# Performance work log

Measured on AMD Instinct MI355X. Metric: run time of the kernel, lower is better.

The kernel has to match this reference:

```python
import jax, jax.numpy as jnp
import numpy as np

V, D, M, R = 100000, 256, 8192, 32
B_SZ, L = 2048, 100


def setup_inputs() -> dict:
    key = jax.random.key(0)
    k1, k2, k3, k4 = jax.random.split(key, 4)
    ids = jax.random.randint(k1, (B_SZ, L), 0, V, dtype=jnp.int64)
    idx = jnp.arange(M, dtype=jnp.int64)  # unique adapter row ids
    E = jax.random.normal(k2, (V, D), dtype=jnp.float32)
    A_rows = jax.random.normal(k3, (M, R), dtype=jnp.float32) * (1.0 / np.sqrt(R))
    Bm = jax.random.normal(k4, (D, R), dtype=jnp.float32) * (1.0 / np.sqrt(R))
    return {"ids": ids, "idx": idx, "E": E, "A_rows": A_rows, "B": Bm}


def reference(ids, idx, E, A_rows, B):
    # base embedding gather: [B, L, D]
    base = E[ids]
    # Equivalent to the one-hot matmul (idx unique): map each vocab id to its
    # adapter-row position, -1 if not adapted.
    pos = jnp.full((V,), -1, dtype=jnp.int32).at[idx].set(
        jnp.arange(idx.shape[0], dtype=jnp.int32))
    p = pos[ids]                      # [B, L]
    hit = (p >= 0)[..., None]         # [B, L, 1]
    A_sel = jnp.where(hit, A_rows[jnp.clip(p, 0)], 0.0)  # [B, L, R]
    delta = jnp.einsum('blr,dr->bld', A_sel, B)           # [B, L, D]
    return base + delta
```

## Files before the change

kernel.cpp:

```cpp
#include <hip/hip_runtime.h>

#define V_SZ   100000
#define D_SZ   256
#define M_SZ   8192
#define R_SZ   32
#define NTOK   (2048 * 100)
#define TPW    8

typedef float f4_t __attribute__((ext_vector_type(4)));

__global__ __launch_bounds__(256) void build_kernel(
    const int*   __restrict__ idx,
    int*         __restrict__ pos,
    const float* __restrict__ E,
    const float* __restrict__ A_rows,
    const float* __restrict__ Bm,
    float*       __restrict__ D2) {

    __shared__ float BtL[R_SZ * D_SZ];

    const int tid = threadIdx.x;

    const int gid = blockIdx.x * 256 + tid;
    if (gid < M_SZ) pos[idx[gid]] = gid;

    for (int f = tid; f < D_SZ * R_SZ; f += 256) {
        BtL[(f & (R_SZ - 1)) * D_SZ + (f >> 5)] = Bm[f];
    }
    __syncthreads();

    const int lane  = tid & 63;
    const int wv    = __builtin_amdgcn_readfirstlane(tid >> 6);
    const int dofs  = lane * 4;
    const int mbase = blockIdx.x * 16 + wv * 4;

    #pragma unroll
    for (int k = 0; k < 4; ++k) {
        const int m   = mbase + k;
        const int row = idx[m];
        const float4 e = *(const float4*)(E + (size_t)row * D_SZ + dofs);
        float ax = 0.f, ay = 0.f, az = 0.f, aw = 0.f;
        #pragma unroll 8
        for (int r = 0; r < R_SZ; ++r) {
            const float  a = A_rows[(size_t)m * R_SZ + r];
            const float4 b = *(const float4*)(BtL + r * D_SZ + dofs);
            ax += a * b.x; ay += a * b.y; az += a * b.z; aw += a * b.w;
        }
        float4 o;
        o.x = e.x + ax; o.y = e.y + ay; o.z = e.z + az; o.w = e.w + aw;
        *(float4*)(D2 + (size_t)m * D_SZ + dofs) = o;
    }
}

__global__ __launch_bounds__(256) void fuse_kernel(
    const int*   __restrict__ ids,
    const float* __restrict__ E,
    const float* __restrict__ D2,
    const int*   __restrict__ pos,
    float*       __restrict__ out) {

    const int lane = threadIdx.x & 63;
    const int wv   = (int)(blockIdx.x * (blockDim.x >> 6) + (threadIdx.x >> 6));
    const int base = wv * TPW;
    const int dofs = lane * 4;

    int myid = 0, myp = -1;
    if (lane < TPW) {
        myid = ids[base + lane];
        myp  = pos[myid];
    }

    float4 e[TPW];
    #pragma unroll
    for (int j = 0; j < TPW; ++j) {
        const int id = __shfl(myid, j);
        const int p  = __shfl(myp,  j);
        const float* src = (p >= 0) ? (D2 + (size_t)p  * D_SZ)
                                    : (E  + (size_t)id * D_SZ);
        e[j] = *(const float4*)(src + dofs);
    }

    #pragma unroll
    for (int j = 0; j < TPW; ++j) {
        f4_t v = { e[j].x, e[j].y, e[j].z, e[j].w };
        __builtin_nontemporal_store(v, (f4_t*)(out + (size_t)(base + j) * D_SZ + dofs));
    }
}


extern "C" void kernel_launch(void* const* d_in, const int* in_sizes, int n_in,
                              void* d_out, int out_size, void* d_ws, size_t ws_size,
                              hipStream_t stream) {
    const int*   ids    = (const int*)  d_in[0];
    const int*   idx    = (const int*)  d_in[1];
    const float* E      = (const float*)d_in[2];
    const float* A_rows = (const float*)d_in[3];
    const float* Bm     = (const float*)d_in[4];
    float*       out    = (float*)      d_out;

    int*   pos = (int*)d_ws;
    size_t pos_bytes = ((size_t)V_SZ * sizeof(int) + 255) & ~(size_t)255;
    float* D2  = (float*)((char*)d_ws + pos_bytes);

    hipLaunchKernelGGL(build_kernel, dim3(512), dim3(256), 0, stream,
                       idx, pos, E, A_rows, Bm, D2);

    hipLaunchKernelGGL(fuse_kernel, dim3(NTOK / (TPW * 4)), dim3(256), 0, stream,
                       ids, E, D2, pos, out);
}
```

Baseline: 313.3 us.

## Precompute token source indices and double-buffer row loads in fuse kernel

```diff
diff --git a/kernel.cpp b/kernel.cpp
--- a/kernel.cpp
+++ b/kernel.cpp
@@ -5,7 +5,8 @@
 #define M_SZ   8192
 #define R_SZ   32
 #define NTOK   (2048 * 100)
-#define TPW    8
+#define TOKW   32
+#define BATCH  8
 
 typedef float f4_t __attribute__((ext_vector_type(4)));
 
@@ -24,18 +25,17 @@
     const int gid = blockIdx.x * 256 + tid;
     if (gid < M_SZ) pos[idx[gid]] = gid;
 
-    for (int f = tid; f < D_SZ * R_SZ; f += 256) {
+    for (int f = tid; f < D_SZ * R_SZ; f += 256)
         BtL[(f & (R_SZ - 1)) * D_SZ + (f >> 5)] = Bm[f];
-    }
     __syncthreads();
 
     const int lane  = tid & 63;
     const int wv    = __builtin_amdgcn_readfirstlane(tid >> 6);
     const int dofs  = lane * 4;
-    const int mbase = blockIdx.x * 16 + wv * 4;
+    const int mbase = blockIdx.x * 64 + wv * 16;
 
-    #pragma unroll
-    for (int k = 0; k < 4; ++k) {
+    #pragma unroll 1
+    for (int k = 0; k < 16; ++k) {
         const int m   = mbase + k;
         const int row = idx[m];
         const float4 e = *(const float4*)(E + (size_t)row * D_SZ + dofs);
@@ -52,39 +52,68 @@
     }
 }
 
+__global__ __launch_bounds__(256) void srcv_kernel(
+    const int* __restrict__ ids,
+    const int* __restrict__ pos,
+    int*       __restrict__ srcv) {
+    const int t4 = blockIdx.x * 256 + threadIdx.x;
+    const int4 id4 = ((const int4*)ids)[t4];
+    int4 o; int p;
+    p = pos[id4.x]; o.x = (p >= 0) ? ~p : id4.x;
+    p = pos[id4.y]; o.y = (p >= 0) ? ~p : id4.y;
+    p = pos[id4.z]; o.z = (p >= 0) ? ~p : id4.z;
+    p = pos[id4.w]; o.w = (p >= 0) ? ~p : id4.w;
+    ((int4*)srcv)[t4] = o;
+}
+
+template <int B>
+__device__ __forceinline__ void load_batch(float4 (&buf)[BATCH], int sv,
+    const float* __restrict__ E, const float* __restrict__ D2, int dofs) {
+    #pragma unroll
+    for (int j = 0; j < BATCH; ++j) {
+        const int s = __builtin_amdgcn_readlane(sv, B * BATCH + j);
+        const float* src = (s < 0) ? (D2 + (size_t)(~s) * D_SZ)
+                                   : (E  + (size_t)s  * D_SZ);
+        buf[j] = *(const float4*)(src + dofs);
+    }
+}
+
+template <int B>
+__device__ __forceinline__ void store_batch(const float4 (&buf)[BATCH],
+    float* __restrict__ obase) {
+    #pragma unroll
+    for (int j = 0; j < BATCH; ++j) {
+        f4_t v = { buf[j].x, buf[j].y, buf[j].z, buf[j].w };
+        __builtin_nontemporal_store(v,
+            (f4_t*)(obase + (size_t)(B * BATCH + j) * D_SZ));
+    }
+}
+
 __global__ __launch_bounds__(256) void fuse_kernel(
-    const int*   __restrict__ ids,
+    const int*   __restrict__ srcv,
     const float* __restrict__ E,
     const float* __restrict__ D2,
-    const int*   __restrict__ pos,
     float*       __restrict__ out) {
 
     const int lane = threadIdx.x & 63;
-    const int wv   = (int)(blockIdx.x * (blockDim.x >> 6) + (threadIdx.x >> 6));
-    const int base = wv * TPW;
+    const int wv   = (int)(blockIdx.x * 4 + (threadIdx.x >> 6));
+    const int base = wv * TOKW;
     const int dofs = lane * 4;
 
-    int myid = 0, myp = -1;
-    if (lane < TPW) {
-        myid = ids[base + lane];
-        myp  = pos[myid];
-    }
+    int sv = 0;
+    if (lane < TOKW) sv = srcv[base + lane];
 
-    float4 e[TPW];
-    #pragma unroll
-    for (int j = 0; j < TPW; ++j) {
-        const int id = __shfl(myid, j);
-        const int p  = __shfl(myp,  j);
-        const float* src = (p >= 0) ? (D2 + (size_t)p  * D_SZ)
-                                    : (E  + (size_t)id * D_SZ);
-        e[j] = *(const float4*)(src + dofs);
-    }
+    float4 eA[BATCH], eB[BATCH];
+    float* const obase = out + (size_t)base * D_SZ + dofs;
 
-    #pragma unroll
-    for (int j = 0; j < TPW; ++j) {
-        f4_t v = { e[j].x, e[j].y, e[j].z, e[j].w };
-        __builtin_nontemporal_store(v, (f4_t*)(out + (size_t)(base + j) * D_SZ + dofs));
-    }
+    load_batch<0>(eA, sv, E, D2, dofs);
+    load_batch<1>(eB, sv, E, D2, dofs);
+    store_batch<0>(eA, obase);
+    load_batch<2>(eA, sv, E, D2, dofs);
+    store_batch<1>(eB, obase);
+    load_batch<3>(eB, sv, E, D2, dofs);
+    store_batch<2>(eA, obase);
+    store_batch<3>(eB, obase);
 }
 
 
@@ -101,10 +130,12 @@
     int*   pos = (int*)d_ws;
     size_t pos_bytes = ((size_t)V_SZ * sizeof(int) + 255) & ~(size_t)255;
     float* D2  = (float*)((char*)d_ws + pos_bytes);
+    int*   srcv = (int*)((char*)d_ws + pos_bytes + (size_t)M_SZ * D_SZ * sizeof(float));
 
-    hipLaunchKernelGGL(build_kernel, dim3(512), dim3(256), 0, stream,
+    hipLaunchKernelGGL(build_kernel, dim3(128), dim3(256), 0, stream,
                        idx, pos, E, A_rows, Bm, D2);
-
-    hipLaunchKernelGGL(fuse_kernel, dim3(NTOK / (TPW * 4)), dim3(256), 0, stream,
-                       ids, E, D2, pos, out);
+    hipLaunchKernelGGL(srcv_kernel, dim3(NTOK / (4 * 256)), dim3(256), 0, stream,
+                       ids, pos, srcv);
+    hipLaunchKernelGGL(fuse_kernel, dim3(NTOK / (TOKW * 4)), dim3(256), 0, stream,
+                       srcv, E, D2, out);
 }
```

Measured after the change: 324.7 us. 3.7% more time.
